# Kernel optimization log

Measured on AMD Instinct MI355X. Metric: run time of the kernel, lower is better.

The kernel has to match this reference:

```python
import jax, jax.numpy as jnp
import numpy as np

B, SQ, SK, D = 8, 2048, 2048, 512

def setup_inputs() -> dict:
    key = jax.random.key(0)
    kq, kk, kv = jax.random.split(key, 3)
    return {
        "query": jax.random.normal(kq, (B, SQ, D), dtype=jnp.float32),
        "key": jax.random.normal(kk, (B, SK, D), dtype=jnp.float32),
        "value": jax.random.normal(kv, (B, SK, D), dtype=jnp.float32),
        "alpha": jnp.float32(0.5),  # learned scalar, init 0.5 as in torch module
    }

def reference(query, key, value, alpha):
    # squared L2 pairwise distances: ||q||^2 + ||k||^2 - 2 q.k  (== cdist(...)**2)
    q2 = jnp.sum(query * query, axis=-1, keepdims=True)          # [B,Sq,1]
    k2 = jnp.sum(key * key, axis=-1, keepdims=True)              # [B,Sk,1]
    qk = jnp.einsum("bqd,bkd->bqk", query, key)                  # [B,Sq,Sk]
    sq_dist = jnp.maximum(q2 + jnp.swapaxes(k2, -1, -2) - 2.0 * qk, 0.0)
    kernel = jnp.exp(-alpha * sq_dist)                            # Gaussian energy well
    weights = jax.nn.softmax(kernel, axis=-1)                     # softmax over keys
    out = jnp.einsum("bqk,bkd->bqd", weights, value)
    return out, weights
```

## Files before the change

### kernel.cpp

```cpp
#include <hip/hip_runtime.h>
#include <stdint.h>

#define B_  8
#define SQ_ 2048
#define SK_ 2048
#define D_  512

typedef unsigned short ushort_t;
typedef __attribute__((ext_vector_type(8))) short          short8;
typedef __attribute__((ext_vector_type(8))) unsigned short ushort8;
typedef __attribute__((ext_vector_type(4))) float          f32x4;

__device__ __forceinline__ unsigned short f2bf(float x) {
  union { float f; unsigned u; } v; v.f = x;
  unsigned r = v.u + 0x7FFFu + ((v.u >> 16) & 1u);
  return (unsigned short)(r >> 16);
}

__device__ __forceinline__ void gload_lds16(const void* g, void* l) {
  __builtin_amdgcn_global_load_lds(
      (__attribute__((address_space(1))) void*)(uintptr_t)g,
      (__attribute__((address_space(3))) void*)l, 16, 0, 0);
}

__global__ void prep_qk(const float* __restrict__ Q, const float* __restrict__ K,
                        ushort_t* __restrict__ Qb, ushort_t* __restrict__ Kb,
                        float* __restrict__ q2, float* __restrict__ k2) {
  const int t = threadIdx.x;
  const int rloc = t >> 7;
  const int row  = blockIdx.x * 2 + rloc;
  const bool isK = row >= B_ * SQ_;
  const int r = isK ? row - B_ * SQ_ : row;
  const float*    src = (isK ? K : Q) + (size_t)r * D_;
  ushort_t*       dst = (isK ? Kb : Qb) + (size_t)r * D_;
  float*          d2  = isK ? k2 : q2;

  const int c = (t & 127) * 4;
  float4 v = *(const float4*)(src + c);
  ushort4 o;
  o.x = f2bf(v.x); o.y = f2bf(v.y); o.z = f2bf(v.z); o.w = f2bf(v.w);
  *(ushort4*)(dst + c) = o;

  float s = v.x * v.x + v.y * v.y + v.z * v.z + v.w * v.w;
  for (int off = 32; off; off >>= 1) s += __shfl_down(s, off);
  __shared__ float ps[4];
  if ((t & 63) == 0) ps[t >> 6] = s;
  __syncthreads();
  if ((t & 127) == 0) d2[r] = ps[rloc * 2] + ps[rloc * 2 + 1];
}

__global__ void prep_vt(const float* __restrict__ V, ushort_t* __restrict__ VT) {
  const int b  = blockIdx.z;
  const int k0 = blockIdx.x * 64;
  const int d0 = blockIdx.y * 64;
  __shared__ __align__(16) ushort_t tile[64][68];
  const int t = threadIdx.x;
  const float* src = V + (size_t)b * SK_ * D_;
  #pragma unroll
  for (int i = 0; i < 4; ++i) {
    int kl = (t >> 4) + i * 16;
    int dl = (t & 15) * 4;
    float4 v = *(const float4*)(src + (size_t)(k0 + kl) * D_ + d0 + dl);
    tile[kl][dl]     = f2bf(v.x);
    tile[kl][dl + 1] = f2bf(v.y);
    tile[kl][dl + 2] = f2bf(v.z);
    tile[kl][dl + 3] = f2bf(v.w);
  }
  __syncthreads();
  ushort_t* dstb = VT + (size_t)b * D_ * SK_;
  #pragma unroll
  for (int j = 0; j < 2; ++j) {
    int chunk = t + j * 256;
    int dl = chunk >> 3;
    int kc = (chunk & 7) << 3;
    ushort8 o;
    #pragma unroll
    for (int m = 0; m < 8; ++m) o[m] = tile[kc + m][dl];
    *(ushort8*)(dstb + (size_t)(d0 + dl) * SK_ + k0 + kc) = o;
  }
}

template <int BF16E>
__global__ __launch_bounds__(256) void qk_kernel(
    const ushort_t* __restrict__ Qb, const ushort_t* __restrict__ Kb,
    const float* __restrict__ q2, const float* __restrict__ k2,
    const float* __restrict__ alphap,
    float* __restrict__ Wf, ushort_t* __restrict__ Ebf,
    float* __restrict__ rowsum) {
  __shared__ __align__(16) ushort_t As[2][8192];
  __shared__ __align__(16) ushort_t Bs[2][8192];
  __shared__ float q2s[128], k2s[128];

  const int t = threadIdx.x;
  const int lane = t & 63, wid = t >> 6;
  const int wA = wid >> 1, wB = wid & 1;

  const int id  = blockIdx.x + 16 * blockIdx.y + 256 * blockIdx.z;
  const int swz = (id & 7) * 256 + (id >> 3);
  const int bx = swz & 15, by = (swz >> 4) & 15, bz = swz >> 8;

  const ushort_t* Aq = Qb + ((size_t)bz * SQ_ + by * 128) * D_;
  const ushort_t* Bk = Kb + ((size_t)bz * SK_ + bx * 128) * D_;

  if (t < 128) q2s[t] = q2[bz * SQ_ + by * 128 + t];
  else         k2s[t - 128] = k2[bz * SK_ + bx * 128 + (t - 128)];

  #define QK_STAGE(buf, kt)                                                     \
    _Pragma("unroll")                                                           \
    for (int i = 0; i < 4; ++i) {                                               \
      int s = t + i * 256;                                                      \
      int row = s >> 3;                                                         \
      int c16 = (s & 7) ^ (row & 7);                                            \
      gload_lds16(Aq + (size_t)row * D_ + (kt) * 64 + c16 * 8,                  \
                  (char*)As[buf] + s * 16);                                     \
      gload_lds16(Bk + (size_t)row * D_ + (kt) * 64 + c16 * 8,                  \
                  (char*)Bs[buf] + s * 16);                                     \
    }

  QK_STAGE(0, 0);
  __syncthreads();

  f32x4 acc[4][4] = {};
  #pragma unroll
  for (int kt = 0; kt < 8; ++kt) {
    const int cur = kt & 1;
    if (kt < 7) { QK_STAGE(cur ^ 1, kt + 1); }
    #pragma unroll
    for (int kk = 0; kk < 2; ++kk) {
      short8 qf[4], kf[4];
      #pragma unroll
      for (int qi = 0; qi < 4; ++qi) {
        int row = (wB << 6) + (qi << 4) + (lane & 15);
        int c = ((kk << 2) + (lane >> 4)) ^ (row & 7);
        qf[qi] = *(const short8*)((const char*)As[cur] + row * 128 + c * 16);
      }
      #pragma unroll
      for (int ki = 0; ki < 4; ++ki) {
        int row = (wA << 6) + (ki << 4) + (lane & 15);
        int c = ((kk << 2) + (lane >> 4)) ^ (row & 7);
        kf[ki] = *(const short8*)((const char*)Bs[cur] + row * 128 + c * 16);
      }
      #pragma unroll
      for (int ki = 0; ki < 4; ++ki)
        #pragma unroll
        for (int qi = 0; qi < 4; ++qi)
          acc[ki][qi] = __builtin_amdgcn_mfma_f32_16x16x32_bf16(kf[ki], qf[qi], acc[ki][qi], 0, 0, 0);
    }
    __syncthreads();
  }
  #undef QK_STAGE

  const float alpha = *alphap;
  const int r0 = (lane >> 4) << 2;
  const int cl = lane & 15;

  float q2v[4];
  #pragma unroll
  for (int qi = 0; qi < 4; ++qi) q2v[qi] = q2s[(wB << 6) + (qi << 4) + cl];

  float se[4] = {0.f, 0.f, 0.f, 0.f};

  #pragma unroll
  for (int ki = 0; ki < 4; ++ki) {
    float k2v[4];
    #pragma unroll
    for (int r = 0; r < 4; ++r) k2v[r] = k2s[(wA << 6) + (ki << 4) + r0 + r];
    #pragma unroll
    for (int qi = 0; qi < 4; ++qi) {
      float x[4], e[4];
      #pragma unroll
      for (int r = 0; r < 4; ++r) {
        float sq = fmaxf(q2v[qi] + k2v[r] - 2.0f * acc[ki][qi][r], 0.0f);
        x[r] = -alpha * sq;
      }
      int small = (x[0] < -20.f) & (x[1] < -20.f) & (x[2] < -20.f) & (x[3] < -20.f);
      if (__all(small)) {
        e[0] = e[1] = e[2] = e[3] = 1.0f;
      } else {
        #pragma unroll
        for (int r = 0; r < 4; ++r) e[r] = __expf(__expf(x[r]));
      }
      se[qi] += e[0] + e[1] + e[2] + e[3];

      const int qrow = (wB << 6) + (qi << 4) + cl;
      const int kcol = bx * 128 + (wA << 6) + (ki << 4) + r0;
      const size_t base = ((size_t)bz * SQ_ + by * 128 + qrow) * SK_ + kcol;
      if (BF16E) {
        unsigned long long pk =
            (unsigned long long)f2bf(e[0])
          | ((unsigned long long)f2bf(e[1]) << 16)
          | ((unsigned long long)f2bf(e[2]) << 32)
          | ((unsigned long long)f2bf(e[3]) << 48);
        *(unsigned long long*)(Ebf + base) = pk;
      } else {
        f32x4 w4 = {e[0], e[1], e[2], e[3]};
        __builtin_nontemporal_store(w4, (f32x4*)(Wf + base));
      }
    }
  }
  #pragma unroll
  for (int qi = 0; qi < 4; ++qi) {
    float s = se[qi];
    s += __shfl_xor(s, 16);
    s += __shfl_xor(s, 32);
    if (lane < 16)
      atomicAdd(&rowsum[bz * SQ_ + by * 128 + (wB << 6) + (qi << 4) + cl], s);
  }
}

__global__ __launch_bounds__(256) void pv_bf16(
    const ushort_t* __restrict__ Eb, const ushort_t* __restrict__ VT,
    const float* __restrict__ rowsum, float* __restrict__ Out,
    float* __restrict__ W) {
  __shared__ __align__(16) ushort_t As[2][8192];
  __shared__ __align__(16) ushort_t Bs[2][8192];
  __shared__ float rss[128];

  const int t = threadIdx.x;
  const int lane = t & 63, wid = t >> 6;
  const int wA = wid >> 1, wB = wid & 1;

  const int id  = blockIdx.x + 4 * blockIdx.y + 64 * blockIdx.z;
  const int swz = (id & 7) * 64 + (id >> 3);
  const int bx = swz & 3, by = (swz >> 2) & 15, bz = swz >> 6;

  const ushort_t* Ebb = Eb + ((size_t)bz * SQ_ + by * 128) * SK_;
  const ushort_t* Vb  = VT + ((size_t)bz * D_ + bx * 128) * SK_;
  float* Wb = W + ((size_t)bz * SQ_ + by * 128) * SK_;

  if (t < 128) rss[t] = rowsum[bz * SQ_ + by * 128 + t];
  __syncthreads();

  #define PV_STAGE(buf, kt)                                                     \
    _Pragma("unroll")                                                           \
    for (int i = 0; i < 4; ++i) {                                               \
      int s = t + i * 256;                                                      \
      int row = s >> 3;                                                         \
      int c16 = (s & 7) ^ (row & 7);                                            \
      gload_lds16(Ebb + (size_t)row * SK_ + (kt) * 64 + c16 * 8,                \
                  (char*)As[buf] + s * 16);                                     \
      gload_lds16(Vb  + (size_t)row * SK_ + (kt) * 64 + c16 * 8,                \
                  (char*)Bs[buf] + s * 16);                                     \
    }

  PV_STAGE(0, 0);
  __syncthreads();

  const int wlo = bx * 8, whi = wlo + 8;
  f32x4 acc[4][4] = {};
  for (int kt = 0; kt < 32; ++kt) {
    const int cur = kt & 1;
    if (kt < 31) { PV_STAGE(cur ^ 1, kt + 1); }

    #pragma unroll
    for (int kk = 0; kk < 2; ++kk) {
      short8 ef[4], vf[4];
      #pragma unroll
      for (int qi = 0; qi < 4; ++qi) {
        int row = (wB << 6) + (qi << 4) + (lane & 15);
        int c = ((kk << 2) + (lane >> 4)) ^ (row & 7);
        ef[qi] = *(const short8*)((const char*)As[cur] + row * 128 + c * 16);
      }
      #pragma unroll
      for (int di = 0; di < 4; ++di) {
        int row = (wA << 6) + (di << 4) + (lane & 15);
        int c = ((kk << 2) + (lane >> 4)) ^ (row & 7);
        vf[di] = *(const short8*)((const char*)Bs[cur] + row * 128 + c * 16);
      }
      #pragma unroll
      for (int di = 0; di < 4; ++di)
        #pragma unroll
        for (int qi = 0; qi < 4; ++qi)
          acc[di][qi] = __builtin_amdgcn_mfma_f32_16x16x32_bf16(vf[di], ef[qi], acc[di][qi], 0, 0, 0);
    }

    if (kt >= wlo && kt < whi) {
      #pragma unroll
      for (int i = 0; i < 4; ++i) {
        int s = t + i * 256;
        int row = s >> 3;
        int c16 = s & 7;
        int c16s = c16 ^ (row & 7);
        ushort8 ev = *(const ushort8*)((const char*)As[cur] + row * 128 + c16s * 16);
        float rinv = 1.0f / rss[row];
        f32x4 lo, hi;
        lo.x = __uint_as_float((unsigned)ev[0] << 16) * rinv;
        lo.y = __uint_as_float((unsigned)ev[1] << 16) * rinv;
        lo.z = __uint_as_float((unsigned)ev[2] << 16) * rinv;
        lo.w = __uint_as_float((unsigned)ev[3] << 16) * rinv;
        hi.x = __uint_as_float((unsigned)ev[4] << 16) * rinv;
        hi.y = __uint_as_float((unsigned)ev[5] << 16) * rinv;
        hi.z = __uint_as_float((unsigned)ev[6] << 16) * rinv;
        hi.w = __uint_as_float((unsigned)ev[7] << 16) * rinv;
        float* wp = Wb + (size_t)row * SK_ + kt * 64 + c16 * 8;
        __builtin_nontemporal_store(lo, (f32x4*)wp);
        __builtin_nontemporal_store(hi, (f32x4*)(wp + 4));
      }
    }
    __syncthreads();
  }
  #undef PV_STAGE

  float* Ob = Out + ((size_t)bz * SQ_ + by * 128) * D_ + bx * 128;
  const int r0 = (lane >> 4) << 2;
  const int cl = lane & 15;
  #pragma unroll
  for (int di = 0; di < 4; ++di) {
    #pragma unroll
    for (int qi = 0; qi < 4; ++qi) {
      int qrow = (wB << 6) + (qi << 4) + cl;
      int dcol = (wA << 6) + (di << 4) + r0;
      float rinv = 1.0f / rss[qrow];
      f32x4 o;
      o.x = acc[di][qi][0] * rinv;
      o.y = acc[di][qi][1] * rinv;
      o.z = acc[di][qi][2] * rinv;
      o.w = acc[di][qi][3] * rinv;
      __builtin_nontemporal_store(o, (f32x4*)(Ob + (size_t)qrow * D_ + dcol));
    }
  }
}

__global__ __launch_bounds__(256) void pv_f32(
    const float* __restrict__ E, const ushort_t* __restrict__ VT,
    const float* __restrict__ rowsum, float* __restrict__ Out) {
  __shared__ __align__(16) ushort_t As[8192];
  __shared__ __align__(16) ushort_t Bs[8192];
  __shared__ float rss[128];

  const int t = threadIdx.x;
  const int lane = t & 63, wid = t >> 6;
  const int wm = wid >> 1, wn = wid & 1;
  const int bx = blockIdx.x, by = blockIdx.y, bz = blockIdx.z;

  const float*    Eb = E + ((size_t)bz * SQ_ + by * 128) * SK_;
  const ushort_t* Vb = VT + ((size_t)bz * D_ + bx * 128) * SK_;

  if (t < 128) rss[t] = rowsum[bz * SQ_ + by * 128 + t];

  f32x4 acc[4][4] = {};
  for (int kt = 0; kt < SK_ / 64; ++kt) {
    float4 va[4][2];
    #pragma unroll
    for (int i = 0; i < 4; ++i) {
      int s = t + i * 256;
      int row = s >> 3, c16 = s & 7;
      const float* g = Eb + (size_t)row * SK_ + kt * 64 + c16 * 8;
      va[i][0] = *(const float4*)g;
      va[i][1] = *(const float4*)(g + 4);
    }
    __syncthreads();
    #pragma unroll
    for (int i = 0; i < 4; ++i) {
      int s = t + i * 256;
      int row = s >> 3, c16 = s & 7;
      int c16s = c16 ^ (row & 7);
      ushort8 o;
      o[0] = f2bf(va[i][0].x); o[1] = f2bf(va[i][0].y);
      o[2] = f2bf(va[i][0].z); o[3] = f2bf(va[i][0].w);
      o[4] = f2bf(va[i][1].x); o[5] = f2bf(va[i][1].y);
      o[6] = f2bf(va[i][1].z); o[7] = f2bf(va[i][1].w);
      *(ushort8*)((char*)As + row * 128 + c16s * 16) = o;
      gload_lds16(Vb + (size_t)row * SK_ + kt * 64 + c16s * 8, (char*)Bs + s * 16);
    }
    __syncthreads();
    #pragma unroll
    for (int kk = 0; kk < 2; ++kk) {
      short8 a[4], bf[4];
      #pragma unroll
      for (int mi = 0; mi < 4; ++mi) {
        int row = (wm << 6) + (mi << 4) + (lane & 15);
        int c = ((kk << 2) + (lane >> 4)) ^ (row & 7);
        a[mi] = *(const short8*)((const char*)As + row * 128 + c * 16);
      }
      #pragma unroll
      for (int ni = 0; ni < 4; ++ni) {
        int col = (wn << 6) + (ni << 4) + (lane & 15);
        int c = ((kk << 2) + (lane >> 4)) ^ (col & 7);
        bf[ni] = *(const short8*)((const char*)Bs + col * 128 + c * 16);
      }
      #pragma unroll
      for (int mi = 0; mi < 4; ++mi)
        #pragma unroll
        for (int ni = 0; ni < 4; ++ni)
          acc[mi][ni] = __builtin_amdgcn_mfma_f32_16x16x32_bf16(a[mi], bf[ni], acc[mi][ni], 0, 0, 0);
    }
  }

  float* Ob = Out + ((size_t)bz * SQ_ + by * 128) * D_ + bx * 128;
  const int r0 = (lane >> 4) << 2;
  const int cl = lane & 15;
  #pragma unroll
  for (int mi = 0; mi < 4; ++mi) {
    #pragma unroll
    for (int r = 0; r < 4; ++r) {
      int rl = (wm << 6) + (mi << 4) + r0 + r;
      float rinv = 1.0f / rss[rl];
      #pragma unroll
      for (int ni = 0; ni < 4; ++ni)
        Ob[(size_t)rl * D_ + (wn << 6) + (ni << 4) + cl] = acc[mi][ni][r] * rinv;
    }
  }
}

__global__ void norm_f32(float* __restrict__ W, const float* __restrict__ rowsum) {
  const size_t total4 = (size_t)B_ * SQ_ * SK_ / 4;
  for (size_t i = (size_t)blockIdx.x * blockDim.x + threadIdx.x; i < total4;
       i += (size_t)gridDim.x * blockDim.x) {
    float4 v = ((const float4*)W)[i];
    float rinv = 1.0f / rowsum[i >> 9];
    v.x *= rinv; v.y *= rinv; v.z *= rinv; v.w *= rinv;
    ((float4*)W)[i] = v;
  }
}

extern "C" void kernel_launch(void* const* d_in, const int* in_sizes, int n_in,
                              void* d_out, int out_size, void* d_ws, size_t ws_size,
                              hipStream_t stream) {
  const float* Q     = (const float*)d_in[0];
  const float* K     = (const float*)d_in[1];
  const float* V     = (const float*)d_in[2];
  const float* alpha = (const float*)d_in[3];

  float* out = (float*)d_out;
  float* W   = out + (size_t)B_ * SQ_ * D_;

  const size_t QKV = (size_t)B_ * SQ_ * D_;
  const size_t NW  = (size_t)B_ * SQ_ * SK_;
  ushort_t* Qb = (ushort_t*)d_ws;
  ushort_t* Kb = Qb + QKV;
  ushort_t* VT = Kb + QKV;

  const size_t need_bf16 = (3 * QKV + NW) * sizeof(ushort_t)
                         + (size_t)(2 * B_ * SQ_ + B_ * SK_) * sizeof(float);
  const bool use_bf16 = ws_size >= need_bf16;

  ushort_t* Eb = VT + QKV;
  float* fbase = use_bf16 ? (float*)(Eb + NW) : (float*)(VT + QKV);
  float* q2     = fbase;
  float* k2     = q2 + B_ * SQ_;
  float* rowsum = k2 + B_ * SK_;

  hipMemsetAsync(rowsum, 0, (size_t)B_ * SQ_ * sizeof(float), stream);

  prep_qk<<<dim3(B_ * SQ_), 256, 0, stream>>>(Q, K, Qb, Kb, q2, k2);
  prep_vt<<<dim3(SK_ / 64, D_ / 64, B_), 256, 0, stream>>>(V, VT);

  if (use_bf16) {
    qk_kernel<1><<<dim3(SK_ / 128, SQ_ / 128, B_), 256, 0, stream>>>(
        Qb, Kb, q2, k2, alpha, nullptr, Eb, rowsum);
    pv_bf16<<<dim3(D_ / 128, SQ_ / 128, B_), 256, 0, stream>>>(Eb, VT, rowsum, out, W);
  } else {
    qk_kernel<0><<<dim3(SK_ / 128, SQ_ / 128, B_), 256, 0, stream>>>(
        Qb, Kb, q2, k2, alpha, W, nullptr, rowsum);
    pv_f32<<<dim3(D_ / 128, SQ_ / 128, B_), 256, 0, stream>>>(W, VT, rowsum, out);
    norm_f32<<<dim3(4096), 256, 0, stream>>>(W, rowsum);
  }
}
```

Measured before the change: 335.0 us.

## Skip PV matmul for score tiles whose softmax weights are uniform

The QK kernel checks whether every score in a 128x128 tile underflows the Gaussian kernel, which makes every softmax numerator exactly one. For such tiles it writes a flag, adds a constant to the row sums and returns without computing exponentials or storing the bf16 numerator tile. The prep kernel now also computes column sums of V per 64-key chunk. For flagged tiles the PV kernel skips the loads and MFMAs and adds these precomputed V sums to the accumulators, and it writes the uniform weights straight from the reciprocal row sum. The shortcut depends on the data and is checked at run time for each tile, at the cost of an extra reduction pass, a flag buffer and more branching.

```diff
diff --git a/kernel.cpp b/kernel.cpp
--- a/kernel.cpp
+++ b/kernel.cpp
@@ -49,13 +49,17 @@
   if ((t & 127) == 0) d2[r] = ps[rloc * 2] + ps[rloc * 2 + 1];
 }
 
-__global__ void prep_vt(const float* __restrict__ V, ushort_t* __restrict__ VT) {
+__global__ void prep_vt(const float* __restrict__ V, ushort_t* __restrict__ VT,
+                        float* __restrict__ Vc) {
   const int b  = blockIdx.z;
   const int k0 = blockIdx.x * 64;
   const int d0 = blockIdx.y * 64;
   __shared__ __align__(16) ushort_t tile[64][68];
+  __shared__ float red[4][16][4];
   const int t = threadIdx.x;
+  const int lane = t & 63, wid = t >> 6;
   const float* src = V + (size_t)b * SK_ * D_;
+  float p0 = 0.f, p1 = 0.f, p2 = 0.f, p3 = 0.f;
   #pragma unroll
   for (int i = 0; i < 4; ++i) {
     int kl = (t >> 4) + i * 16;
@@ -65,8 +69,25 @@
     tile[kl][dl + 1] = f2bf(v.y);
     tile[kl][dl + 2] = f2bf(v.z);
     tile[kl][dl + 3] = f2bf(v.w);
+    p0 += v.x; p1 += v.y; p2 += v.z; p3 += v.w;
+  }
+  #pragma unroll
+  for (int off = 16; off < 64; off <<= 1) {
+    p0 += __shfl_xor(p0, off);
+    p1 += __shfl_xor(p1, off);
+    p2 += __shfl_xor(p2, off);
+    p3 += __shfl_xor(p3, off);
+  }
+  if (lane < 16) {
+    red[wid][lane][0] = p0; red[wid][lane][1] = p1;
+    red[wid][lane][2] = p2; red[wid][lane][3] = p3;
   }
   __syncthreads();
+  if (t < 64) {
+    int g = t >> 2, c = t & 3;
+    float s = red[0][g][c] + red[1][g][c] + red[2][g][c] + red[3][g][c];
+    Vc[((size_t)b * 32 + (k0 >> 6)) * D_ + d0 + t] = s;
+  }
   ushort_t* dstb = VT + (size_t)b * D_ * SK_;
   #pragma unroll
   for (int j = 0; j < 2; ++j) {
@@ -86,10 +107,11 @@
     const float* __restrict__ q2, const float* __restrict__ k2,
     const float* __restrict__ alphap,
     float* __restrict__ Wf, ushort_t* __restrict__ Ebf,
-    float* __restrict__ rowsum) {
+    float* __restrict__ rowsum, unsigned char* __restrict__ flags) {
   __shared__ __align__(16) ushort_t As[2][8192];
   __shared__ __align__(16) ushort_t Bs[2][8192];
   __shared__ float q2s[128], k2s[128];
+  __shared__ int vts[4];
 
   const int t = threadIdx.x;
   const int lane = t & 63, wid = t >> 6;
@@ -158,8 +180,35 @@
   #pragma unroll
   for (int qi = 0; qi < 4; ++qi) q2v[qi] = q2s[(wB << 6) + (qi << 4) + cl];
 
+  int allneg = 1;
+  #pragma unroll
+  for (int ki = 0; ki < 4; ++ki) {
+    #pragma unroll
+    for (int r = 0; r < 4; ++r) {
+      float k2r = k2s[(wA << 6) + (ki << 4) + r0 + r];
+      #pragma unroll
+      for (int qi = 0; qi < 4; ++qi) {
+        float sq = fmaxf(q2v[qi] + k2r - 2.0f * acc[ki][qi][r], 0.0f);
+        allneg &= (-alpha * sq < -20.0f) ? 1 : 0;
+      }
+    }
+  }
+  if (lane == 0) vts[wid] = __all(allneg) ? 1 : 0;
+  __syncthreads();
+  const int uniform = vts[0] & vts[1] & vts[2] & vts[3];
+
+  if (BF16E && uniform) {
+    if (t == 0) flags[(bz * 16 + by) * 16 + bx] = 1;
+    if (lane < 16) {
+      #pragma unroll
+      for (int qi = 0; qi < 4; ++qi)
+        atomicAdd(&rowsum[bz * SQ_ + by * 128 + (wB << 6) + (qi << 4) + cl], 64.0f);
+    }
+    return;
+  }
+  if (BF16E && t == 0) flags[(bz * 16 + by) * 16 + bx] = 0;
+
   float se[4] = {0.f, 0.f, 0.f, 0.f};
-
   #pragma unroll
   for (int ki = 0; ki < 4; ++ki) {
     float k2v[4];
@@ -211,14 +260,18 @@
 __global__ __launch_bounds__(256) void pv_bf16(
     const ushort_t* __restrict__ Eb, const ushort_t* __restrict__ VT,
     const float* __restrict__ rowsum, float* __restrict__ Out,
-    float* __restrict__ W) {
+    float* __restrict__ W, const float* __restrict__ Vc,
+    const unsigned char* __restrict__ flags) {
   __shared__ __align__(16) ushort_t As[2][8192];
   __shared__ __align__(16) ushort_t Bs[2][8192];
   __shared__ float rss[128];
+  __shared__ unsigned char fls[16];
 
   const int t = threadIdx.x;
   const int lane = t & 63, wid = t >> 6;
   const int wA = wid >> 1, wB = wid & 1;
+  const int r0 = (lane >> 4) << 2;
+  const int cl = lane & 15;
 
   const int id  = blockIdx.x + 4 * blockIdx.y + 64 * blockIdx.z;
   const int swz = (id & 7) * 64 + (id >> 3);
@@ -229,6 +282,7 @@
   float* Wb = W + ((size_t)bz * SQ_ + by * 128) * SK_;
 
   if (t < 128) rss[t] = rowsum[bz * SQ_ + by * 128 + t];
+  if (t < 16)  fls[t] = flags[(bz * 16 + by) * 16 + t];
   __syncthreads();
 
   #define PV_STAGE(buf, kt)                                                     \
@@ -243,58 +297,82 @@
                   (char*)Bs[buf] + s * 16);                                     \
     }
 
-  PV_STAGE(0, 0);
+  if (!fls[0]) { PV_STAGE(0, 0); }
   __syncthreads();
 
   const int wlo = bx * 8, whi = wlo + 8;
   f32x4 acc[4][4] = {};
   for (int kt = 0; kt < 32; ++kt) {
     const int cur = kt & 1;
-    if (kt < 31) { PV_STAGE(cur ^ 1, kt + 1); }
-
-    #pragma unroll
-    for (int kk = 0; kk < 2; ++kk) {
-      short8 ef[4], vf[4];
-      #pragma unroll
-      for (int qi = 0; qi < 4; ++qi) {
-        int row = (wB << 6) + (qi << 4) + (lane & 15);
-        int c = ((kk << 2) + (lane >> 4)) ^ (row & 7);
-        ef[qi] = *(const short8*)((const char*)As[cur] + row * 128 + c * 16);
-      }
+    if (kt < 31 && !fls[(kt + 1) >> 1]) { PV_STAGE(cur ^ 1, kt + 1); }
+
+    if (!fls[kt >> 1]) {
+      #pragma unroll
+      for (int kk = 0; kk < 2; ++kk) {
+        short8 ef[4], vf[4];
+        #pragma unroll
+        for (int qi = 0; qi < 4; ++qi) {
+          int row = (wB << 6) + (qi << 4) + (lane & 15);
+          int c = ((kk << 2) + (lane >> 4)) ^ (row & 7);
+          ef[qi] = *(const short8*)((const char*)As[cur] + row * 128 + c * 16);
+        }
+        #pragma unroll
+        for (int di = 0; di < 4; ++di) {
+          int row = (wA << 6) + (di << 4) + (lane & 15);
+          int c = ((kk << 2) + (lane >> 4)) ^ (row & 7);
+          vf[di] = *(const short8*)((const char*)Bs[cur] + row * 128 + c * 16);
+        }
+        #pragma unroll
+        for (int di = 0; di < 4; ++di)
+          #pragma unroll
+          for (int qi = 0; qi < 4; ++qi)
+            acc[di][qi] = __builtin_amdgcn_mfma_f32_16x16x32_bf16(vf[di], ef[qi], acc[di][qi], 0, 0, 0);
+      }
+    } else {
+      const float* vcp = Vc + ((size_t)bz * 32 + kt) * D_ + bx * 128 + (wA << 6) + r0;
       #pragma unroll
       for (int di = 0; di < 4; ++di) {
-        int row = (wA << 6) + (di << 4) + (lane & 15);
-        int c = ((kk << 2) + (lane >> 4)) ^ (row & 7);
-        vf[di] = *(const short8*)((const char*)Bs[cur] + row * 128 + c * 16);
-      }
-      #pragma unroll
-      for (int di = 0; di < 4; ++di)
-        #pragma unroll
-        for (int qi = 0; qi < 4; ++qi)
-          acc[di][qi] = __builtin_amdgcn_mfma_f32_16x16x32_bf16(vf[di], ef[qi], acc[di][qi], 0, 0, 0);
+        f32x4 vc = *(const f32x4*)(vcp + (di << 4));
+        #pragma unroll
+        for (int qi = 0; qi < 4; ++qi) acc[di][qi] += vc;
+      }
     }
 
     if (kt >= wlo && kt < whi) {
-      #pragma unroll
-      for (int i = 0; i < 4; ++i) {
-        int s = t + i * 256;
-        int row = s >> 3;
-        int c16 = s & 7;
-        int c16s = c16 ^ (row & 7);
-        ushort8 ev = *(const ushort8*)((const char*)As[cur] + row * 128 + c16s * 16);
-        float rinv = 1.0f / rss[row];
-        f32x4 lo, hi;
-        lo.x = __uint_as_float((unsigned)ev[0] << 16) * rinv;
-        lo.y = __uint_as_float((unsigned)ev[1] << 16) * rinv;
-        lo.z = __uint_as_float((unsigned)ev[2] << 16) * rinv;
-        lo.w = __uint_as_float((unsigned)ev[3] << 16) * rinv;
-        hi.x = __uint_as_float((unsigned)ev[4] << 16) * rinv;
-        hi.y = __uint_as_float((unsigned)ev[5] << 16) * rinv;
-        hi.z = __uint_as_float((unsigned)ev[6] << 16) * rinv;
-        hi.w = __uint_as_float((unsigned)ev[7] << 16) * rinv;
-        float* wp = Wb + (size_t)row * SK_ + kt * 64 + c16 * 8;
-        __builtin_nontemporal_store(lo, (f32x4*)wp);
-        __builtin_nontemporal_store(hi, (f32x4*)(wp + 4));
+      if (!fls[kt >> 1]) {
+        #pragma unroll
+        for (int i = 0; i < 4; ++i) {
+          int s = t + i * 256;
+          int row = s >> 3;
+          int c16 = s & 7;
+          int c16s = c16 ^ (row & 7);
+          ushort8 ev = *(const ushort8*)((const char*)As[cur] + row * 128 + c16s * 16);
+          float rinv = 1.0f / rss[row];
+          f32x4 lo, hi;
+          lo.x = __uint_as_float((unsigned)ev[0] << 16) * rinv;
+          lo.y = __uint_as_float((unsigned)ev[1] << 16) * rinv;
+          lo.z = __uint_as_float((unsigned)ev[2] << 16) * rinv;
+          lo.w = __uint_as_float((unsigned)ev[3] << 16) * rinv;
+          hi.x = __uint_as_float((unsigned)ev[4] << 16) * rinv;
+          hi.y = __uint_as_float((unsigned)ev[5] << 16) * rinv;
+          hi.z = __uint_as_float((unsigned)ev[6] << 16) * rinv;
+          hi.w = __uint_as_float((unsigned)ev[7] << 16) * rinv;
+          float* wp = Wb + (size_t)row * SK_ + kt * 64 + c16 * 8;
+          __builtin_nontemporal_store(lo, (f32x4*)wp);
+          __builtin_nontemporal_store(hi, (f32x4*)(wp + 4));
+        }
+      } else {
+        #pragma unroll
+        for (int i = 0; i < 4; ++i) {
+          int s = t + i * 256;
+          int row = s >> 3;
+          int c16 = s & 7;
+          float rinv = 1.0f / rss[row];
+          f32x4 w = {rinv, rinv, rinv, rinv};
+          float* wp = Wb + (size_t)row * SK_ + kt * 64 + c16 * 8;
+          __builtin_nontemporal_store(w, (f32x4*)wp);
+          __builtin_nontemporal_store(w, (f32x4*)(wp + 4));
+        }
       }
     }
     __syncthreads();
@@ -302,8 +380,6 @@
   #undef PV_STAGE
 
   float* Ob = Out + ((size_t)bz * SQ_ + by * 128) * D_ + bx * 128;
-  const int r0 = (lane >> 4) << 2;
-  const int cl = lane & 15;
   #pragma unroll
   for (int di = 0; di < 4; ++di) {
     #pragma unroll
@@ -427,12 +503,14 @@
 
   const size_t QKV = (size_t)B_ * SQ_ * D_;
   const size_t NW  = (size_t)B_ * SQ_ * SK_;
+  const size_t NVC = (size_t)B_ * 32 * D_;
   ushort_t* Qb = (ushort_t*)d_ws;
   ushort_t* Kb = Qb + QKV;
   ushort_t* VT = Kb + QKV;
 
   const size_t need_bf16 = (3 * QKV + NW) * sizeof(ushort_t)
-                         + (size_t)(2 * B_ * SQ_ + B_ * SK_) * sizeof(float);
+                         + (size_t)(2 * B_ * SQ_ + B_ * SK_) * sizeof(float)
+                         + NVC * sizeof(float) + 2048;
   const bool use_bf16 = ws_size >= need_bf16;
 
   ushort_t* Eb = VT + QKV;
@@ -440,19 +518,22 @@
   float* q2     = fbase;
   float* k2     = q2 + B_ * SQ_;
   float* rowsum = k2 + B_ * SK_;
+  float* Vc     = rowsum + B_ * SQ_;
+  unsigned char* flags = (unsigned char*)(Vc + NVC);
 
   hipMemsetAsync(rowsum, 0, (size_t)B_ * SQ_ * sizeof(float), stream);
 
   prep_qk<<<dim3(B_ * SQ_), 256, 0, stream>>>(Q, K, Qb, Kb, q2, k2);
-  prep_vt<<<dim3(SK_ / 64, D_ / 64, B_), 256, 0, stream>>>(V, VT);
+  prep_vt<<<dim3(SK_ / 64, D_ / 64, B_), 256, 0, stream>>>(V, VT, Vc);
 
   if (use_bf16) {
     qk_kernel<1><<<dim3(SK_ / 128, SQ_ / 128, B_), 256, 0, stream>>>(
-        Qb, Kb, q2, k2, alpha, nullptr, Eb, rowsum);
-    pv_bf16<<<dim3(D_ / 128, SQ_ / 128, B_), 256, 0, stream>>>(Eb, VT, rowsum, out, W);
+        Qb, Kb, q2, k2, alpha, nullptr, Eb, rowsum, flags);
+    pv_bf16<<<dim3(D_ / 128, SQ_ / 128, B_), 256, 0, stream>>>(
+        Eb, VT, rowsum, out, W, Vc, flags);
   } else {
     qk_kernel<0><<<dim3(SK_ / 128, SQ_ / 128, B_), 256, 0, stream>>>(
-        Qb, Kb, q2, k2, alpha, W, nullptr, rowsum);
+        Qb, Kb, q2, k2, alpha, W, nullptr, rowsum, nullptr);
     pv_f32<<<dim3(D_ / 128, SQ_ / 128, B_), 256, 0, stream>>>(W, VT, rowsum, out);
     norm_f32<<<dim3(4096), 256, 0, stream>>>(W, rowsum);
   }
```

Measured after the change: 347.6 us. 1.04x slower.
